# Optimization experiments

Hardware: AMD Instinct MI355X
Metric: run time of the kernel (lower is better)

## Reference

```python
import jax, jax.numpy as jnp
import numpy as np

VOCAB, D_W, H, S, B = 50000, 300, 128, 256, 128
NUM_CAP, DIM_CAP, ROUTINGS, EPS = 10, 16, 5, 1e-7

def setup_inputs() -> dict:
    key = jax.random.key(0)
    ks = jax.random.split(key, 12)
    sc = lambda *sh: 1.0 / np.sqrt(sh[-1])
    inp = {
        "x": jax.random.randint(ks[0], (B, S), 0, VOCAB),
        "emb": jax.random.normal(ks[1], (VOCAB, D_W), jnp.float32),
        # GRU params, PyTorch gate order (r,z,n), forward and backward directions
        "w_ih_f": jax.random.normal(ks[2], (3 * H, D_W), jnp.float32) * sc(D_W),
        "w_hh_f": jax.random.normal(ks[3], (3 * H, H), jnp.float32) * sc(H),
        "b_ih_f": jnp.zeros((3 * H,), jnp.float32),
        "b_hh_f": jnp.zeros((3 * H,), jnp.float32),
        "w_ih_b": jax.random.normal(ks[4], (3 * H, D_W), jnp.float32) * sc(D_W),
        "w_hh_b": jax.random.normal(ks[5], (3 * H, H), jnp.float32) * sc(H),
        "b_ih_b": jnp.zeros((3 * H,), jnp.float32),
        "b_hh_b": jnp.zeros((3 * H,), jnp.float32),
        "W_cap": jax.random.normal(ks[6], (2 * H, NUM_CAP * DIM_CAP), jnp.float32) * sc(2 * H),
        "W_lin": jax.random.normal(ks[7], (NUM_CAP * DIM_CAP, 2), jnp.float32) * sc(NUM_CAP * DIM_CAP),
        "b_lin": jnp.zeros((2,), jnp.float32),
    }
    return inp

def _gru_dir(xs, w_ih, w_hh, b_ih, b_hh, reverse):
    # xs: [S, B, D] -> hidden states [S, B, H]
    x_proj = jnp.einsum('sbd,gd->sbg', xs, w_ih) + b_ih  # [S,B,3H]
    h0 = jnp.zeros((xs.shape[1], w_hh.shape[1]), xs.dtype)
    def step(h, xp):
        hp = h @ w_hh.T + b_hh
        xr, xz, xn = jnp.split(xp, 3, axis=-1)
        hr, hz, hn = jnp.split(hp, 3, axis=-1)
        r = jax.nn.sigmoid(xr + hr)
        z = jax.nn.sigmoid(xz + hz)
        n = jnp.tanh(xn + r * hn)
        h_new = (1.0 - z) * n + z * h
        return h_new, h_new
    _, hs = jax.lax.scan(step, h0, x_proj, reverse=reverse)
    return hs

def _squash(v, axis=-1):
    # note: source 'squash' is pure L2-normalization with eps (no n^2/(1+n^2) factor)
    s = jnp.sum(v * v, axis=axis, keepdims=True)
    return v / jnp.sqrt(s + EPS)

def _capsule(h, W_cap):
    # h: [B, S, 2H]
    u_hat = jnp.einsum('bsd,dm->bsm', h, W_cap)  # [B,S,NC*DC]
    u_hat = u_hat.reshape(h.shape[0], h.shape[1], NUM_CAP, DIM_CAP)
    u_hat = jnp.transpose(u_hat, (0, 2, 1, 3))  # [B, NC, S, DC]
    b = jnp.zeros(u_hat.shape[:3], u_hat.dtype)  # [B, NC, S]
    outputs = None
    for i in range(ROUTINGS):
        c = jax.nn.softmax(b, axis=1)  # softmax over capsules
        outputs = _squash(jnp.einsum('bij,bijk->bik', c, u_hat))  # [B, NC, DC]
        if i < ROUTINGS - 1:
            b = b + jnp.einsum('bik,bijk->bij', outputs, u_hat)
    return outputs

def reference(x, emb, w_ih_f, w_hh_f, b_ih_f, b_hh_f,
              w_ih_b, w_hh_b, b_ih_b, b_hh_b, W_cap, W_lin, b_lin):
    e = emb[x]  # [B, S, D_W]; dropout is identity in eval mode
    xs = jnp.transpose(e, (1, 0, 2))  # [S, B, D]
    hf = _gru_dir(xs, w_ih_f, w_hh_f, b_ih_f, b_hh_f, reverse=False)
    hb = _gru_dir(xs, w_ih_b, w_hh_b, b_ih_b, b_hh_b, reverse=True)
    h = jnp.transpose(jnp.concatenate([hf, hb], axis=-1), (1, 0, 2))  # [B,S,2H]
    caps = _capsule(h, W_cap)  # [B, NC, DC]
    flat = caps.reshape(caps.shape[0], -1)  # [B, 160]
    return flat @ W_lin + b_lin
```

## Files before the change

kernel.cpp:

```cpp
#include <hip/hip_runtime.h>
#include <cmath>

#define DW 300
#define HH 128
#define G3 384
#define GN 768
#define SS 256
#define NB 128
#define NC 10
#define DC 16
#define NCDC 160
#define CAP_EPS 1e-7f
#define KP 320

typedef _Float16 h8v __attribute__((ext_vector_type(8)));
typedef _Float16 h4v __attribute__((ext_vector_type(4)));
typedef float f32x4 __attribute__((ext_vector_type(4)));

__device__ __forceinline__ float rcp_(float x) { return __builtin_amdgcn_rcpf(x); }
__device__ __forceinline__ float sigmoidf_(float x) {
  return rcp_(1.0f + __expf(-x));
}
__device__ __forceinline__ float tanhf_(float x) {
  return 1.0f - 2.0f * rcp_(__expf(2.0f * x) + 1.0f);
}
__device__ __forceinline__ void bar_lds() {
  asm volatile("s_waitcnt lgkmcnt(0)\n\ts_barrier" ::: "memory");
}

__global__ __launch_bounds__(64) void k0_prep(
    const int* __restrict__ x, const float* __restrict__ emb,
    const float* __restrict__ wif, const float* __restrict__ wib,
    const float* __restrict__ Wc,
    _Float16* __restrict__ A16, _Float16* __restrict__ Bw16,
    _Float16* __restrict__ WcT)
{
  const int row = blockIdx.x;
  const int t = threadIdx.x;
  if (row < 33536) {
    const float* __restrict__ src;
    _Float16* __restrict__ dst;
    if (row < 32768) {
      src = emb + (size_t)x[(row & 127) * SS + (row >> 7)] * DW;
      dst = A16 + (size_t)row * KP;
    } else {
      const int n = row - 32768;
      src = (n < G3) ? (wif + (size_t)n * DW) : (wib + (size_t)(n - G3) * DW);
      dst = Bw16 + (size_t)n * KP;
    }
#pragma unroll
    for (int p = 0; p < 2; ++p) {
      const int idx = p * 64 + t;
      if (idx < 75) {
        const float4 v = *(const float4*)(src + idx * 4);
        h4v o = {(_Float16)v.x, (_Float16)v.y, (_Float16)v.z, (_Float16)v.w};
        *(h4v*)(dst + idx * 4) = o;
      }
    }
    if (t < 5) {
      h4v z = {(_Float16)0.f, (_Float16)0.f, (_Float16)0.f, (_Float16)0.f};
      *(h4v*)(dst + 300 + t * 4) = z;
    }
  } else {
    const int n = row - 33536;
    _Float16* __restrict__ dst = WcT + (size_t)n * 256;
#pragma unroll
    for (int p = 0; p < 4; ++p) {
      const int k = p * 64 + t;
      dst[k] = (_Float16)Wc[(size_t)k * NCDC + n];
    }
  }
}

__global__ __launch_bounds__(256) void k1_xproj(
    const _Float16* __restrict__ A16, const _Float16* __restrict__ Bw16,
    const float* __restrict__ bf, const float* __restrict__ bb,
    _Float16* __restrict__ xp16)
{
  __shared__ __align__(16) _Float16 Asb[128 * 64];
  __shared__ __align__(16) _Float16 Bsb[128 * 64];
  __shared__ __align__(16) _Float16 Ls[128 * 132];
  const int tid = threadIdx.x;
  const int s_idx = blockIdx.x;
  const int n0 = blockIdx.y * 128;
  const int m0 = s_idx * 128;
  const int dir = (n0 >= G3) ? 1 : 0;
  const int G = (n0 >> 7) - dir * 3;

  const int lane = tid & 63;
  const int wv = tid >> 6, wm = wv >> 1, wn = wv & 1;
  const int fr = lane & 15, kc4 = lane >> 4;

  const int srow = tid >> 3;
  const int sch  = tid & 7;

  f32x4 acc[4][4];
#pragma unroll
  for (int i = 0; i < 4; ++i)
#pragma unroll
    for (int j = 0; j < 4; ++j) acc[i][j] = (f32x4){0.f, 0.f, 0.f, 0.f};

  h8v ra[4], rb[4];
#pragma unroll
  for (int i = 0; i < 4; ++i) {
    const int r = i * 32 + srow;
    ra[i] = *(const h8v*)(A16 + (size_t)(m0 + r) * KP + sch * 8);
    rb[i] = *(const h8v*)(Bw16 + (size_t)(n0 + r) * KP + sch * 8);
  }

  for (int kt = 0; kt < 5; ++kt) {
    if (kt) bar_lds();
#pragma unroll
    for (int i = 0; i < 4; ++i) {
      const int r = i * 32 + srow;
      const int off = (r * 128 + sch * 16) ^ ((r & 7) << 4);
      *(h8v*)((char*)Asb + off) = ra[i];
      *(h8v*)((char*)Bsb + off) = rb[i];
    }
    if (kt < 4) {
      const int kb = (kt + 1) * 64;
#pragma unroll
      for (int i = 0; i < 4; ++i) {
        const int r = i * 32 + srow;
        ra[i] = *(const h8v*)(A16 + (size_t)(m0 + r) * KP + kb + sch * 8);
        rb[i] = *(const h8v*)(Bw16 + (size_t)(n0 + r) * KP + kb + sch * 8);
      }
    }
    bar_lds();

    h8v af[4][2], bfv[4][2];
#pragma unroll
    for (int mf = 0; mf < 4; ++mf) {
      const int rA = wm * 64 + mf * 16 + fr;
#pragma unroll
      for (int ks = 0; ks < 2; ++ks) {
        const int off = (rA * 128 + ks * 64 + kc4 * 16) ^ ((rA & 7) << 4);
        af[mf][ks] = *(const h8v*)((const char*)Asb + off);
      }
    }
#pragma unroll
    for (int nf = 0; nf < 4; ++nf) {
      const int rB = wn * 64 + nf * 16 + fr;
#pragma unroll
      for (int ks = 0; ks < 2; ++ks) {
        const int off = (rB * 128 + ks * 64 + kc4 * 16) ^ ((rB & 7) << 4);
        bfv[nf][ks] = *(const h8v*)((const char*)Bsb + off);
      }
    }
#pragma unroll
    for (int ks = 0; ks < 2; ++ks)
#pragma unroll
      for (int mf = 0; mf < 4; ++mf)
#pragma unroll
        for (int nf = 0; nf < 4; ++nf)
          acc[mf][nf] = __builtin_amdgcn_mfma_f32_16x16x32_f16(
              af[mf][ks], bfv[nf][ks], acc[mf][nf], 0, 0, 0);
  }

  const float* __restrict__ bsrc = (n0 < G3) ? (bf + n0) : (bb + (n0 - G3));
  float bval[4];
#pragma unroll
  for (int nf = 0; nf < 4; ++nf) bval[nf] = bsrc[wn * 64 + nf * 16 + fr];

#pragma unroll
  for (int mf = 0; mf < 4; ++mf)
#pragma unroll
    for (int e = 0; e < 4; ++e) {
      const int r = wm * 64 + mf * 16 + kc4 * 4 + e;
#pragma unroll
      for (int nf = 0; nf < 4; ++nf) {
        const int c = wn * 64 + nf * 16 + fr;
        Ls[r * 132 + c] = (_Float16)(acc[mf][nf][e] + bval[nf]);
      }
    }
  __syncthreads();

  {
    const int r = tid >> 1;
    const int hf = tid & 1;
    _Float16* __restrict__ dst =
        xp16 + ((size_t)(dir * NB + r) * SS + s_idx) * G3 + G * 128 + hf * 64;
    const _Float16* srcl = &Ls[r * 132 + hf * 64];
#pragma unroll
    for (int i = 0; i < 8; ++i)
      *(h8v*)(dst + i * 8) = *(const h8v*)(srcl + i * 8);
  }
}

__global__ __launch_bounds__(512) void k2_gru(
    const _Float16* __restrict__ xp16,
    const float* __restrict__ whf, const float* __restrict__ whb,
    const float* __restrict__ bhf, const float* __restrict__ bhb,
    _Float16* __restrict__ hcat16)
{
  const int blk = blockIdx.x;
  const int dir = blk >> 7;
  const int b   = blk & 127;
  const int tid = threadIdx.x;
  const int jg  = tid >> 6;
  const int lane = tid & 63;
  const int fr = lane & 15;
  const int qq = lane >> 4;

  const float* __restrict__ wh = dir ? whb : whf;
  const float* __restrict__ bh = dir ? bhb : bhf;

  h8v wB[3][4];
  float bias_[3];
#pragma unroll
  for (int G = 0; G < 3; ++G) {
    const int row = G * HH + jg * 16 + fr;
    const float* __restrict__ p = wh + (size_t)row * HH;
#pragma unroll
    for (int kc = 0; kc < 4; ++kc) {
      const float* q = p + kc * 32 + qq * 8;
      const float4 u0 = *(const float4*)(q);
      const float4 u1 = *(const float4*)(q + 4);
      wB[G][kc] = (h8v){(_Float16)u0.x, (_Float16)u0.y, (_Float16)u0.z,
                        (_Float16)u0.w, (_Float16)u1.x, (_Float16)u1.y,
                        (_Float16)u1.z, (_Float16)u1.w};
    }
    bias_[G] = bh[G * HH + jg * 16 + fr];
  }

  __shared__ __align__(16) _Float16 h16[HH];
  if (tid < 16) *(h8v*)(h16 + tid * 8) = (h8v){0, 0, 0, 0, 0, 0, 0, 0};
  __syncthreads();

  const int stp = dir ? -1 : 1;
  int s = dir ? (SS - 1) : 0;
  const ptrdiff_t xstp = (ptrdiff_t)stp * G3;
  const ptrdiff_t hstp = (ptrdiff_t)stp * 256;
  const _Float16* __restrict__ xptr =
      xp16 + (size_t)(dir * NB + b) * SS * G3 + (size_t)s * G3;
  _Float16* __restrict__ hptr =
      hcat16 + ((size_t)b * SS + s) * 256 + dir * HH;

  _Float16 xv[3];
#pragma unroll
  for (int G = 0; G < 3; ++G)
    xv[G] = xptr[G * 128 + jg * 16 + fr];

  float hold = 0.f;

  for (int it = 0; it < SS; ++it) {
    h8v afr[4];
#pragma unroll
    for (int kc = 0; kc < 4; ++kc)
      afr[kc] = *(const h8v*)((const char*)h16 + kc * 64 + qq * 16);

    float xc[3];
#pragma unroll
    for (int G = 0; G < 3; ++G) xc[G] = (float)xv[G];
    if (it < SS - 1) {
      xptr += xstp;
#pragma unroll
      for (int G = 0; G < 3; ++G)
        xv[G] = xptr[G * 128 + jg * 16 + fr];
    }

    f32x4 acc[3];
    acc[0] = (f32x4){xc[0] + bias_[0], 0.f, 0.f, 0.f};
    acc[1] = (f32x4){xc[1] + bias_[1], 0.f, 0.f, 0.f};
    acc[2] = (f32x4){bias_[2], 0.f, 0.f, 0.f};
#pragma unroll
    for (int G = 0; G < 3; ++G)
#pragma unroll
      for (int kc = 0; kc < 4; ++kc)
        acc[G] = __builtin_amdgcn_mfma_f32_16x16x32_f16(
            afr[kc], wB[G][kc], acc[G], 0, 0, 0);

    bar_lds();

    const float r = sigmoidf_(acc[0][0]);
    const float z = sigmoidf_(acc[1][0]);
    const float n = tanhf_(xc[2] + r * acc[2][0]);
    const float hnew = (1.f - z) * n + z * hold;
    hold = hnew;
    if (qq == 0) {
      const int j = jg * 16 + fr;
      const _Float16 hv = (_Float16)hnew;
      h16[j] = hv;
      hptr[j] = hv;
    }
    hptr += hstp;
    bar_lds();
  }
}

__global__ __launch_bounds__(256) void k3_uhat(
    const _Float16* __restrict__ hcat16, const _Float16* __restrict__ WcT,
    float* __restrict__ uh)
{
  __shared__ __align__(16) _Float16 Hs[128 * 256];
  const int tid = threadIdx.x;
  const int m0 = blockIdx.x * 128;
  const int lane = tid & 63, wv = tid >> 6;
  const int fr = lane & 15, qq = lane >> 4;

  const int srow = tid >> 5;
  const int sch  = tid & 31;
#pragma unroll
  for (int i = 0; i < 16; ++i) {
    const int r = i * 8 + srow;
    const h8v v = *(const h8v*)(hcat16 + (size_t)(m0 + r) * 256 + sch * 8);
    const int off = (r * 512 + sch * 16) ^ ((r & 7) << 4);
    *(h8v*)((char*)Hs + off) = v;
  }
  __syncthreads();

  f32x4 acc[2][10];
#pragma unroll
  for (int mt = 0; mt < 2; ++mt)
#pragma unroll
    for (int nt = 0; nt < 10; ++nt) acc[mt][nt] = (f32x4){0.f, 0.f, 0.f, 0.f};

#pragma unroll
  for (int kc = 0; kc < 8; ++kc) {
    h8v bf_[10];
#pragma unroll
    for (int nt = 0; nt < 10; ++nt)
      bf_[nt] = *(const h8v*)(WcT + (size_t)(nt * 16 + fr) * 256 + kc * 32 + qq * 8);
    h8v af[2];
#pragma unroll
    for (int mt = 0; mt < 2; ++mt) {
      const int rA = wv * 32 + mt * 16 + fr;
      const int off = (rA * 512 + kc * 64 + qq * 16) ^ ((rA & 7) << 4);
      af[mt] = *(const h8v*)((const char*)Hs + off);
    }
#pragma unroll
    for (int mt = 0; mt < 2; ++mt)
#pragma unroll
      for (int nt = 0; nt < 10; ++nt)
        acc[mt][nt] = __builtin_amdgcn_mfma_f32_16x16x32_f16(
            af[mt], bf_[nt], acc[mt][nt], 0, 0, 0);
  }

#pragma unroll
  for (int mt = 0; mt < 2; ++mt)
#pragma unroll
    for (int nt = 0; nt < 10; ++nt)
#pragma unroll
      for (int e = 0; e < 4; ++e) {
        const int m = m0 + wv * 32 + mt * 16 + qq * 4 + e;
        uh[(size_t)m * NCDC + nt * 16 + fr] = acc[mt][nt][e];
      }
}

__global__ __launch_bounds__(256) void k4_route(
    const float* __restrict__ uhat, const float* __restrict__ Wl,
    const float* __restrict__ bl, float* __restrict__ outp)
{
  const int b = blockIdx.x;
  const int t = threadIdx.x;
  __shared__ float blog[NC][SS + 1];
  __shared__ float cbuf[NC][SS + 1];
  __shared__ float vout[NC][DC];
  __shared__ float red0[256], red1[256];

  const float* __restrict__ u = uhat + (size_t)b * SS * NCDC;

#pragma unroll
  for (int i = 0; i < NC; ++i) blog[i][t] = 0.f;
  __syncthreads();

  const int ci = t >> 4, ck = t & 15;
  float myval = 0.f;

  for (int it = 0; it < 5; ++it) {
    float m = blog[0][t];
#pragma unroll
    for (int i = 1; i < NC; ++i) m = fmaxf(m, blog[i][t]);
    float e[NC];
    float sum = 0.f;
#pragma unroll
    for (int i = 0; i < NC; ++i) { e[i] = __expf(blog[i][t] - m); sum += e[i]; }
    const float inv = __builtin_amdgcn_rcpf(sum);
#pragma unroll
    for (int i = 0; i < NC; ++i) cbuf[i][t] = e[i] * inv;
    __syncthreads();

    if (t < NCDC) {
      float acc = 0.f;
#pragma unroll 4
      for (int jj = 0; jj < SS; ++jj)
        acc += cbuf[ci][jj] * u[(size_t)jj * NCDC + t];
      float ss = acc * acc;
      ss += __shfl_xor(ss, 1);
      ss += __shfl_xor(ss, 2);
      ss += __shfl_xor(ss, 4);
      ss += __shfl_xor(ss, 8);
      myval = acc * __builtin_amdgcn_rsqf(ss + CAP_EPS);
      vout[ci][ck] = myval;
    }
    __syncthreads();

    if (it < 4) {
      const float* ur = u + (size_t)t * NCDC;
#pragma unroll
      for (int i = 0; i < NC; ++i) {
        float dot = 0.f;
#pragma unroll
        for (int k = 0; k < DC; ++k) dot += ur[i * DC + k] * vout[i][k];
        blog[i][t] += dot;
      }
      __syncthreads();
    }
  }

  float p0 = 0.f, p1 = 0.f;
  if (t < NCDC) { p0 = myval * Wl[2 * t]; p1 = myval * Wl[2 * t + 1]; }
  red0[t] = p0; red1[t] = p1;
  __syncthreads();
  for (int off = 128; off >= 1; off >>= 1) {
    if (t < off) { red0[t] += red0[t + off]; red1[t] += red1[t + off]; }
    __syncthreads();
  }
  if (t == 0) {
    outp[2 * b + 0] = red0[0] + bl[0];
    outp[2 * b + 1] = red1[0] + bl[1];
  }
}

extern "C" void kernel_launch(void* const* d_in, const int* in_sizes, int n_in,
                              void* d_out, int out_size, void* d_ws, size_t ws_size,
                              hipStream_t stream) {
  (void)in_sizes; (void)n_in; (void)out_size; (void)ws_size;
  const int*   x    = (const int*)  d_in[0];
  const float* emb  = (const float*)d_in[1];
  const float* wif  = (const float*)d_in[2];
  const float* whf  = (const float*)d_in[3];
  const float* bif  = (const float*)d_in[4];
  const float* bhf  = (const float*)d_in[5];
  const float* wib  = (const float*)d_in[6];
  const float* whb  = (const float*)d_in[7];
  const float* bib  = (const float*)d_in[8];
  const float* bhb  = (const float*)d_in[9];
  const float* Wc   = (const float*)d_in[10];
  const float* Wl   = (const float*)d_in[11];
  const float* bl   = (const float*)d_in[12];
  float* out = (float*)d_out;

  char* base = (char*)d_ws;
  _Float16* xp16   = (_Float16*)base;
  _Float16* hcat16 = (_Float16*)(base + 50331648);
  float*    uh     = (float*)   (base + 67108864);
  _Float16* A16    = (_Float16*)(base + 88080384);
  _Float16* Bw16   = (_Float16*)(base + 109051904);
  _Float16* WcT    = (_Float16*)(base + 109543424);

  hipLaunchKernelGGL(k0_prep, dim3(33696), dim3(64), 0, stream,
                     x, emb, wif, wib, Wc, A16, Bw16, WcT);
  hipLaunchKernelGGL(k1_xproj, dim3(256, 6), dim3(256), 0, stream,
                     A16, Bw16, bif, bib, xp16);
  hipLaunchKernelGGL(k2_gru, dim3(256), dim3(512), 0, stream,
                     xp16, whf, whb, bhf, bhb, hcat16);
  hipLaunchKernelGGL(k3_uhat, dim3(256), dim3(256), 0, stream,
                     hcat16, WcT, uh);
  hipLaunchKernelGGL(k4_route, dim3(128), dim3(256), 0, stream,
                     uh, Wl, bl, out);
}
```

Before: 252.1 us.

## Store u_hat in fp16 and cache per-token rows in registers for routing

```diff
diff --git a/kernel.cpp b/kernel.cpp
--- a/kernel.cpp
+++ b/kernel.cpp
@@ -290,7 +290,7 @@
 
 __global__ __launch_bounds__(256) void k3_uhat(
     const _Float16* __restrict__ hcat16, const _Float16* __restrict__ WcT,
-    float* __restrict__ uh)
+    _Float16* __restrict__ uh16)
 {
   __shared__ __align__(16) _Float16 Hs[128 * 256];
   const int tid = threadIdx.x;
@@ -336,29 +336,60 @@
             af[mt], bf_[nt], acc[mt][nt], 0, 0, 0);
   }
 
+  __syncthreads();
 #pragma unroll
   for (int mt = 0; mt < 2; ++mt)
 #pragma unroll
     for (int nt = 0; nt < 10; ++nt)
 #pragma unroll
       for (int e = 0; e < 4; ++e) {
-        const int m = m0 + wv * 32 + mt * 16 + qq * 4 + e;
-        uh[(size_t)m * NCDC + nt * 16 + fr] = acc[mt][nt][e];
-      }
+        const int ml = wv * 32 + mt * 16 + qq * 4 + e;
+        Hs[ml * 168 + nt * 16 + fr] = (_Float16)acc[mt][nt][e];
+      }
+  __syncthreads();
+  {
+    const int row = tid >> 1;
+    const int hf  = tid & 1;
+    _Float16* __restrict__ dst = uh16 + (size_t)(m0 + row) * NCDC + hf * 80;
+    const _Float16* srcl = &Hs[row * 168 + hf * 80];
+#pragma unroll
+    for (int i = 0; i < 10; ++i)
+      *(h8v*)(dst + i * 8) = *(const h8v*)(srcl + i * 8);
+  }
 }
 
 __global__ __launch_bounds__(256) void k4_route(
-    const float* __restrict__ uhat, const float* __restrict__ Wl,
+    const _Float16* __restrict__ uh16, const float* __restrict__ Wl,
     const float* __restrict__ bl, float* __restrict__ outp)
 {
   const int b = blockIdx.x;
   const int t = threadIdx.x;
+  __shared__ __align__(16) _Float16 stage[64 * 168];
   __shared__ float blog[NC][SS + 1];
   __shared__ float cbuf[NC][SS + 1];
   __shared__ float vout[NC][DC];
   __shared__ float red0[256], red1[256];
 
-  const float* __restrict__ u = uhat + (size_t)b * SS * NCDC;
+  const _Float16* __restrict__ src = uh16 + (size_t)b * SS * NCDC;
+
+  h4v urow[40];
+  for (int chunk = 0; chunk < 4; ++chunk) {
+    for (int idx = t; idx < 64 * 20; idx += 256) {
+      const int r = idx / 20, c8 = idx % 20;
+      const h8v v = *(const h8v*)(src + (size_t)(chunk * 64 + r) * NCDC + c8 * 8);
+      _Float16* d = &stage[r * 168 + c8 * 8];
+      *(h4v*)(d)     = (h4v){v[0], v[1], v[2], v[3]};
+      *(h4v*)(d + 4) = (h4v){v[4], v[5], v[6], v[7]};
+    }
+    __syncthreads();
+    if ((t >> 6) == chunk) {
+      const int r = t & 63;
+#pragma unroll
+      for (int q = 0; q < 40; ++q)
+        urow[q] = *(const h4v*)(&stage[r * 168 + q * 4]);
+    }
+    __syncthreads();
+  }
 
 #pragma unroll
   for (int i = 0; i < NC; ++i) blog[i][t] = 0.f;
@@ -381,10 +412,13 @@
     __syncthreads();
 
     if (t < NCDC) {
-      float acc = 0.f;
-#pragma unroll 4
-      for (int jj = 0; jj < SS; ++jj)
-        acc += cbuf[ci][jj] * u[(size_t)jj * NCDC + t];
+      float acc0 = 0.f, acc1 = 0.f;
+#pragma unroll 8
+      for (int jj = 0; jj < SS; jj += 2) {
+        acc0 += cbuf[ci][jj] * (float)src[(size_t)jj * NCDC + t];
+        acc1 += cbuf[ci][jj + 1] * (float)src[(size_t)(jj + 1) * NCDC + t];
+      }
+      const float acc = acc0 + acc1;
       float ss = acc * acc;
       ss += __shfl_xor(ss, 1);
       ss += __shfl_xor(ss, 2);
@@ -396,12 +430,17 @@
     __syncthreads();
 
     if (it < 4) {
-      const float* ur = u + (size_t)t * NCDC;
 #pragma unroll
       for (int i = 0; i < NC; ++i) {
         float dot = 0.f;
 #pragma unroll
-        for (int k = 0; k < DC; ++k) dot += ur[i * DC + k] * vout[i][k];
+        for (int q = 0; q < 4; ++q) {
+          const h4v u4 = urow[i * 4 + q];
+          dot += (float)u4[0] * vout[i][q * 4 + 0]
+               + (float)u4[1] * vout[i][q * 4 + 1]
+               + (float)u4[2] * vout[i][q * 4 + 2]
+               + (float)u4[3] * vout[i][q * 4 + 3];
+        }
         blog[i][t] += dot;
       }
       __syncthreads();
@@ -444,7 +483,7 @@
   char* base = (char*)d_ws;
   _Float16* xp16   = (_Float16*)base;
   _Float16* hcat16 = (_Float16*)(base + 50331648);
-  float*    uh     = (float*)   (base + 67108864);
+  _Float16* uh16   = (_Float16*)(base + 67108864);
   _Float16* A16    = (_Float16*)(base + 88080384);
   _Float16* Bw16   = (_Float16*)(base + 109051904);
   _Float16* WcT    = (_Float16*)(base + 109543424);
@@ -456,7 +495,7 @@
   hipLaunchKernelGGL(k2_gru, dim3(256), dim3(512), 0, stream,
                      xp16, whf, whb, bhf, bhb, hcat16);
   hipLaunchKernelGGL(k3_uhat, dim3(256), dim3(256), 0, stream,
-                     hcat16, WcT, uh);
+                     hcat16, WcT, uh16);
   hipLaunchKernelGGL(k4_route, dim3(128), dim3(256), 0, stream,
-                     uh, Wl, bl, out);
-}
+                     uh16, Wl, bl, out);
+}
```

Result: faster. 217.7 us (-13.6%).
